# Optimization experiments

Hardware: AMD Instinct MI355X
Metric: run time of the kernel (lower is better)

The kernel has to match this reference:

```python
import jax, jax.numpy as jnp
import numpy as np

H = 1024   # hidden_dim
B = 4096   # batch
T = 128    # forecast_len
IN = 1     # output_dim (univariate)


def setup_inputs() -> dict:
    key = jax.random.key(0)
    ks = jax.random.split(key, 8)
    s = 1.0 / np.sqrt(H)  # torch LSTM/Linear default uniform init scale
    u = lambda k, shape: jax.random.uniform(k, shape, jnp.float32, -s, s)
    return {
        "hidden": jax.random.normal(ks[0], (1, B, H), jnp.float32),
        "cell":   jax.random.normal(ks[1], (1, B, H), jnp.float32),
        "W_ih":   u(ks[2], (4 * H, IN)),   # torch gate order: i, f, g, o
        "W_hh":   u(ks[3], (4 * H, H)),
        "b_ih":   u(ks[4], (4 * H,)),
        "b_hh":   u(ks[5], (4 * H,)),
        "W_out":  u(ks[6], (IN, H)),
        "b_out":  u(ks[7], (IN,)),
    }


def reference(hidden, cell, W_ih, W_hh, b_ih, b_hh, W_out, b_out):
    h = hidden[0]  # [B, H]  (num_layers == 1)
    c = cell[0]    # [B, H]
    x0 = jnp.zeros((h.shape[0], IN), h.dtype)  # initial decoder input = zeros
    b = b_ih + b_hh

    def step(carry, _):
        x, h, c = carry
        gates = x @ W_ih.T + h @ W_hh.T + b          # [B, 4H]
        i, f, g, o = jnp.split(gates, 4, axis=-1)    # torch order i,f,g,o
        c = jax.nn.sigmoid(f) * c + jax.nn.sigmoid(i) * jnp.tanh(g)
        h = jax.nn.sigmoid(o) * jnp.tanh(c)
        pred = h @ W_out.T + b_out                   # [B, 1]
        return (pred, h, c), pred                    # prediction fed back as next input

    _, preds = jax.lax.scan(step, (x0, h, c), None, length=T)  # [T, B, 1]
    return jnp.transpose(preds, (1, 0, 2))  # [B, T, 1]
```

## Files before the change

kernel.cpp:

```cpp
#include <hip/hip_runtime.h>
#include <hip/hip_bf16.h>
#include <stdint.h>


#define HH 1024
#define BB 4096
#define TT 128

#define BM 128
#define BN 256
#define BKK 32
#define NTIL 32

typedef __bf16 bf16;
typedef __bf16 v8bf __attribute__((ext_vector_type(8)));
typedef float f32x4 __attribute__((ext_vector_type(4)));

__device__ __forceinline__ float fast_sigmoid(float x) {
    return 1.0f / (1.0f + __expf(-x));
}
__device__ __forceinline__ float fast_tanh(float x) {
    return 1.0f - 2.0f / (__expf(2.0f * x) + 1.0f);
}

__device__ __forceinline__ void gload_lds16(const void* g, void* l) {
    __builtin_amdgcn_global_load_lds(
        (const __attribute__((address_space(1))) uint32_t*)(uintptr_t)g,
        (__attribute__((address_space(3))) uint32_t*)(uint32_t)(uintptr_t)l,
        16, 0, 0);
}

#define FENCE() asm volatile("" ::: "memory")
#define BAR() do { FENCE(); __builtin_amdgcn_s_barrier(); FENCE(); } while (0)
#define WAITV0() asm volatile("s_waitcnt vmcnt(0)" ::: "memory")
#define WAITV6() asm volatile("s_waitcnt vmcnt(6)" ::: "memory")
#define WAITL0() asm volatile("s_waitcnt lgkmcnt(0)" ::: "memory")


__global__ void prep_weights(const float* __restrict__ Whh,
                             const float* __restrict__ bih,
                             const float* __restrict__ bhh,
                             const float* __restrict__ Wih,
                             const float* __restrict__ Wout,
                             const float* __restrict__ bout,
                             bf16* __restrict__ Wr0, bf16* __restrict__ Wr1,
                             float* __restrict__ bias0, float* __restrict__ bias1) {
    int idx = blockIdx.x * blockDim.x + threadIdx.x;
    if (idx < 4 * HH * HH) {
        int k   = idx & (HH - 1);
        int row = idx >> 10;
        int jb2 = row >> 8;
        int g   = (row >> 6) & 3;
        int jj  = row & 63;
        int srow = g * HH + jb2 * 64 + jj;
        float wv = Whh[srow * HH + k];
        Wr0[idx] = (bf16)wv;
        Wr1[idx] = (bf16)(wv + Wih[srow] * Wout[k]);
    }
    if (idx < 4 * HH) {
        float b = bih[idx] + bhh[idx];
        bias0[idx] = b;
        bias1[idx] = b + Wih[idx] * bout[0];
    }
}

__global__ void prep_h(const float* __restrict__ h0, bf16* __restrict__ hb) {
    int idx = blockIdx.x * blockDim.x + threadIdx.x;
    if (idx < BB * HH) hb[idx] = (bf16)h0[idx];
}

__global__ void prep_c(const float* __restrict__ c0, bf16* __restrict__ cb) {
    int idx = blockIdx.x * blockDim.x + threadIdx.x;
    if (idx < BB * HH) cb[idx] = (bf16)c0[idx];
}

__global__ void prep_pred(float* __restrict__ predbuf, const float* __restrict__ b_out) {
    int idx = blockIdx.x * blockDim.x + threadIdx.x;
    if (idx < (TT + 1) * BB) predbuf[idx] = b_out[0];
}


#define STAGE1(SrcL, dstArr, TGT, ldsRowBase, KN)                              \
    gload_lds16((SrcL) + (size_t)(2 * (ldsRowBase)) * HH + (KN),               \
                &dstArr[TGT][ldsRowBase][0]);

#define READ_FRAGS(BUF)                                                        \
    _Pragma("unroll")                                                          \
    for (int mi = 0; mi < 4; mi++)                                             \
        a[mi] = *(const v8bf*)&As[BUF][waveM * 32 + mi * 8 + rh][pA];          \
    _Pragma("unroll")                                                          \
    for (int g = 0; g < 4; g++)                                                \
        _Pragma("unroll")                                                      \
        for (int jh = 0; jh < 2; jh++)                                         \
            b[g * 2 + jh] = *(const v8bf*)                                     \
                &Bs[BUF][g * 32 + waveN * 16 + jh * 8 + rh][pA];

#define MFMA_ALL()                                                             \
    __builtin_amdgcn_s_setprio(1);                                             \
    _Pragma("unroll")                                                          \
    for (int mi = 0; mi < 4; mi++)                                             \
        _Pragma("unroll")                                                      \
        for (int nt = 0; nt < 8; nt++)                                         \
            acc[mi][nt] = __builtin_amdgcn_mfma_f32_16x16x32_bf16(             \
                a[mi], b[nt], acc[mi][nt], 0, 0, 0);                           \
    __builtin_amdgcn_s_setprio(0);

#define TILE_BODY(BUF, TGT, T)                                                 \
    {                                                                          \
        v8bf a[4], b[8];                                                       \
        if ((T) < NTIL - 2) {                                                  \
            const int kn_ = ((T) + 2) * BKK;                                   \
            _Pragma("unroll")                                                  \
            for (int c2 = 0; c2 < 2; c2++)                                     \
                STAGE1(AsrcL, As, TGT, w * 16 + c2 * 8, kn_)                   \
            _Pragma("unroll")                                                  \
            for (int c2 = 0; c2 < 4; c2++)                                     \
                STAGE1(BsrcL, Bs, TGT, w * 32 + c2 * 8, kn_)                   \
        }                                                                      \
        READ_FRAGS(BUF)                                                        \
        MFMA_ALL()                                                             \
        WAITL0();                                                              \
        if ((T) < NTIL - 2) { WAITV6(); } else { WAITV0(); }                   \
        BAR();                                                                 \
    }

__global__ __launch_bounds__(256, 2)
void lstm_step(const bf16* __restrict__ hread, bf16* __restrict__ hwrite,
               bf16* __restrict__ cbuf,
               const bf16* __restrict__ Wr, const float* __restrict__ biasp,
               const float* __restrict__ Wout, float* __restrict__ predbuf_w) {
    __shared__ __align__(16) bf16 As[3][64][64];
    __shared__ __align__(16) bf16 Bs[3][128][64];

    const int tid   = threadIdx.x;
    const int lane  = tid & 63;
    const int w     = tid >> 6;
    const int waveM = w >> 1, waveN = w & 1;
    const int quad  = lane >> 4, l15 = lane & 15;

    const int bid    = blockIdx.x;
    const int jb2    = (bid & 7) * 2 + ((bid >> 3) & 1);
    const int blockB = (bid >> 4) * BM;

    const bf16* Asrc = hread + (size_t)blockB * HH;
    const bf16* Bsrc = Wr + (size_t)jb2 * 256 * HH;

    const int t1  = (lane & 7) ^ (lane >> 3);
    const int grl = 2 * (lane >> 3) + (t1 >> 2);
    const int c8  = (t1 & 3) * 8;
    const bf16* AsrcL = Asrc + (size_t)grl * HH + c8;
    const bf16* BsrcL = Bsrc + (size_t)grl * HH + c8;

    const int rh = l15 >> 1;
    const int pA = (((quad + 4 * (l15 & 1)) ^ rh)) * 8;

    float bsvv[2][4], wov[2];
#pragma unroll
    for (int jh = 0; jh < 2; jh++) {
        const int j = jb2 * 64 + waveN * 32 + jh * 16 + l15;
#pragma unroll
        for (int g = 0; g < 4; g++) bsvv[jh][g] = biasp[g * HH + j];
        wov[jh] = Wout[j];
    }

    f32x4 acc[4][8];
#pragma unroll
    for (int mi = 0; mi < 4; mi++)
#pragma unroll
        for (int g = 0; g < 4; g++)
#pragma unroll
            for (int jh = 0; jh < 2; jh++) {
                const float bv = bsvv[jh][g];
                acc[mi][g * 2 + jh] = (f32x4){bv, bv, bv, bv};
            }

#pragma unroll
    for (int c2 = 0; c2 < 2; c2++) STAGE1(AsrcL, As, 0, w * 16 + c2 * 8, 0)
#pragma unroll
    for (int c2 = 0; c2 < 4; c2++) STAGE1(BsrcL, Bs, 0, w * 32 + c2 * 8, 0)
#pragma unroll
    for (int c2 = 0; c2 < 2; c2++) STAGE1(AsrcL, As, 1, w * 16 + c2 * 8, BKK)
#pragma unroll
    for (int c2 = 0; c2 < 4; c2++) STAGE1(BsrcL, Bs, 1, w * 32 + c2 * 8, BKK)
    WAITV6();
    BAR();

#pragma unroll 1
    for (int tt = 0; tt < 10; tt++) {
        TILE_BODY(0, 2, 3 * tt)
        TILE_BODY(1, 0, 3 * tt + 1)
        TILE_BODY(2, 1, 3 * tt + 2)
    }
    TILE_BODY(0, 2, 30)
    TILE_BODY(1, 0, 31)

#pragma unroll
    for (int mi = 0; mi < 4; mi++) {
#pragma unroll
        for (int r = 0; r < 4; r++) {
            const int b = blockB + waveM * 64 + mi * 16 + quad * 4 + r;
            float pacc = 0.0f;
#pragma unroll
            for (int jh = 0; jh < 2; jh++) {
                const int j = jb2 * 64 + waveN * 32 + jh * 16 + l15;
                const float gi = acc[mi][0 + jh][r];
                const float gf = acc[mi][2 + jh][r];
                const float gg = acc[mi][4 + jh][r];
                const float go = acc[mi][6 + jh][r];
                const float cprev = (float)cbuf[(size_t)b * HH + j];
                const float cn = fast_sigmoid(gf) * cprev
                               + fast_sigmoid(gi) * fast_tanh(gg);
                cbuf[(size_t)b * HH + j] = (bf16)cn;
                const float hn = fast_sigmoid(go) * fast_tanh(cn);
                hwrite[(size_t)b * HH + j] = (bf16)hn;
                pacc += hn * wov[jh];
            }
            pacc += __shfl_xor(pacc, 1);
            pacc += __shfl_xor(pacc, 2);
            pacc += __shfl_xor(pacc, 4);
            pacc += __shfl_xor(pacc, 8);
            if (l15 == 0) atomicAdd(&predbuf_w[b], pacc);
        }
    }
}


__global__ void write_out(const float* __restrict__ predbuf, float* __restrict__ out) {
    int idx = blockIdx.x * blockDim.x + threadIdx.x;
    if (idx < BB * TT) {
        int t = idx & (TT - 1);
        int b = idx >> 7;
        out[idx] = predbuf[(size_t)(t + 1) * BB + b];
    }
}


extern "C" void kernel_launch(void* const* d_in, const int* in_sizes, int n_in,
                              void* d_out, int out_size, void* d_ws, size_t ws_size,
                              hipStream_t stream) {
    const float* hidden = (const float*)d_in[0];
    const float* cell   = (const float*)d_in[1];
    const float* Wih    = (const float*)d_in[2];
    const float* Whh    = (const float*)d_in[3];
    const float* bih    = (const float*)d_in[4];
    const float* bhh    = (const float*)d_in[5];
    const float* Wout   = (const float*)d_in[6];
    const float* bout   = (const float*)d_in[7];
    float* out = (float*)d_out;

    char* ws = (char*)d_ws;
    bf16* Wr0 = (bf16*)ws;       ws += (size_t)4 * HH * HH * 2;
    bf16* Wr1 = (bf16*)ws;       ws += (size_t)4 * HH * HH * 2;
    bf16* hb0 = (bf16*)ws;       ws += (size_t)BB * HH * 2;
    bf16* hb1 = (bf16*)ws;       ws += (size_t)BB * HH * 2;
    bf16* cbuf = (bf16*)ws;      ws += (size_t)BB * HH * 2;
    float* bias0 = (float*)ws;   ws += (size_t)4 * HH * 4;
    float* bias1 = (float*)ws;   ws += (size_t)4 * HH * 4;
    float* predbuf = (float*)ws; ws += (size_t)(TT + 1) * BB * 4;

    prep_weights<<<(4 * HH * HH + 255) / 256, 256, 0, stream>>>(
        Whh, bih, bhh, Wih, Wout, bout, Wr0, Wr1, bias0, bias1);
    prep_h<<<(BB * HH + 255) / 256, 256, 0, stream>>>(hidden, hb0);
    prep_c<<<(BB * HH + 255) / 256, 256, 0, stream>>>(cell, cbuf);
    prep_pred<<<((TT + 1) * BB + 255) / 256, 256, 0, stream>>>(predbuf, bout);

    bf16* hb[2] = {hb0, hb1};
    for (int t = 0; t < TT; t++) {
        const bf16* hr = hb[t & 1];
        bf16* hw = hb[(t + 1) & 1];
        const bf16* Wr   = (t == 0) ? Wr0 : Wr1;
        const float* bsp = (t == 0) ? bias0 : bias1;
        lstm_step<<<512, 256, 0, stream>>>(
            hr, hw, cbuf, Wr, bsp, Wout, predbuf + (size_t)(t + 1) * BB);
    }

    write_out<<<(BB * TT + 255) / 256, 256, 0, stream>>>(predbuf, out);
}
```

Baseline: 5.745 ms.

## Replace triple-buffered K pipeline with single-buffer BK=64 loop and new block mapping

```diff
diff --git a/kernel.cpp b/kernel.cpp
--- a/kernel.cpp
+++ b/kernel.cpp
@@ -8,9 +8,7 @@
 #define TT 128
 
 #define BM 128
-#define BN 256
-#define BKK 32
-#define NTIL 32
+#define BKK 64
 
 typedef __bf16 bf16;
 typedef __bf16 v8bf __attribute__((ext_vector_type(8)));
@@ -29,12 +27,6 @@
         (__attribute__((address_space(3))) uint32_t*)(uint32_t)(uintptr_t)l,
         16, 0, 0);
 }
-
-#define FENCE() asm volatile("" ::: "memory")
-#define BAR() do { FENCE(); __builtin_amdgcn_s_barrier(); FENCE(); } while (0)
-#define WAITV0() asm volatile("s_waitcnt vmcnt(0)" ::: "memory")
-#define WAITV6() asm volatile("s_waitcnt vmcnt(6)" ::: "memory")
-#define WAITL0() asm volatile("s_waitcnt lgkmcnt(0)" ::: "memory")
 
 
 __global__ void prep_weights(const float* __restrict__ Whh,
@@ -80,57 +72,13 @@
 }
 
 
-#define STAGE1(SrcL, dstArr, TGT, ldsRowBase, KN)                              \
-    gload_lds16((SrcL) + (size_t)(2 * (ldsRowBase)) * HH + (KN),               \
-                &dstArr[TGT][ldsRowBase][0]);
-
-#define READ_FRAGS(BUF)                                                        \
-    _Pragma("unroll")                                                          \
-    for (int mi = 0; mi < 4; mi++)                                             \
-        a[mi] = *(const v8bf*)&As[BUF][waveM * 32 + mi * 8 + rh][pA];          \
-    _Pragma("unroll")                                                          \
-    for (int g = 0; g < 4; g++)                                                \
-        _Pragma("unroll")                                                      \
-        for (int jh = 0; jh < 2; jh++)                                         \
-            b[g * 2 + jh] = *(const v8bf*)                                     \
-                &Bs[BUF][g * 32 + waveN * 16 + jh * 8 + rh][pA];
-
-#define MFMA_ALL()                                                             \
-    __builtin_amdgcn_s_setprio(1);                                             \
-    _Pragma("unroll")                                                          \
-    for (int mi = 0; mi < 4; mi++)                                             \
-        _Pragma("unroll")                                                      \
-        for (int nt = 0; nt < 8; nt++)                                         \
-            acc[mi][nt] = __builtin_amdgcn_mfma_f32_16x16x32_bf16(             \
-                a[mi], b[nt], acc[mi][nt], 0, 0, 0);                           \
-    __builtin_amdgcn_s_setprio(0);
-
-#define TILE_BODY(BUF, TGT, T)                                                 \
-    {                                                                          \
-        v8bf a[4], b[8];                                                       \
-        if ((T) < NTIL - 2) {                                                  \
-            const int kn_ = ((T) + 2) * BKK;                                   \
-            _Pragma("unroll")                                                  \
-            for (int c2 = 0; c2 < 2; c2++)                                     \
-                STAGE1(AsrcL, As, TGT, w * 16 + c2 * 8, kn_)                   \
-            _Pragma("unroll")                                                  \
-            for (int c2 = 0; c2 < 4; c2++)                                     \
-                STAGE1(BsrcL, Bs, TGT, w * 32 + c2 * 8, kn_)                   \
-        }                                                                      \
-        READ_FRAGS(BUF)                                                        \
-        MFMA_ALL()                                                             \
-        WAITL0();                                                              \
-        if ((T) < NTIL - 2) { WAITV6(); } else { WAITV0(); }                   \
-        BAR();                                                                 \
-    }
-
 __global__ __launch_bounds__(256, 2)
 void lstm_step(const bf16* __restrict__ hread, bf16* __restrict__ hwrite,
                bf16* __restrict__ cbuf,
                const bf16* __restrict__ Wr, const float* __restrict__ biasp,
                const float* __restrict__ Wout, float* __restrict__ predbuf_w) {
-    __shared__ __align__(16) bf16 As[3][64][64];
-    __shared__ __align__(16) bf16 Bs[3][128][64];
+    __shared__ bf16 As[BM][BKK];
+    __shared__ bf16 Bs[2 * BM][BKK];
 
     const int tid   = threadIdx.x;
     const int lane  = tid & 63;
@@ -138,21 +86,17 @@
     const int waveM = w >> 1, waveN = w & 1;
     const int quad  = lane >> 4, l15 = lane & 15;
 
-    const int bid    = blockIdx.x;
-    const int jb2    = (bid & 7) * 2 + ((bid >> 3) & 1);
-    const int blockB = (bid >> 4) * BM;
+    const int bid = blockIdx.x;
+    const int xcd = bid & 7, loc = bid >> 3;
+    const int jb2 = (xcd & 3) * 4 + (loc & 3);
+    const int blockB = ((xcd >> 2) * 16 + (loc >> 2)) * BM;
 
     const bf16* Asrc = hread + (size_t)blockB * HH;
     const bf16* Bsrc = Wr + (size_t)jb2 * 256 * HH;
 
-    const int t1  = (lane & 7) ^ (lane >> 3);
-    const int grl = 2 * (lane >> 3) + (t1 >> 2);
-    const int c8  = (t1 & 3) * 8;
-    const bf16* AsrcL = Asrc + (size_t)grl * HH + c8;
-    const bf16* BsrcL = Bsrc + (size_t)grl * HH + c8;
-
-    const int rh = l15 >> 1;
-    const int pA = (((quad + 4 * (l15 & 1)) ^ rh)) * 8;
+    const int r8  = lane >> 3;
+    const int gc  = (lane & 7) ^ r8;
+    const int swr = l15 & 7;
 
     float bsvv[2][4], wov[2];
 #pragma unroll
@@ -174,25 +118,41 @@
                 acc[mi][g * 2 + jh] = (f32x4){bv, bv, bv, bv};
             }
 
-#pragma unroll
-    for (int c2 = 0; c2 < 2; c2++) STAGE1(AsrcL, As, 0, w * 16 + c2 * 8, 0)
-#pragma unroll
-    for (int c2 = 0; c2 < 4; c2++) STAGE1(BsrcL, Bs, 0, w * 32 + c2 * 8, 0)
-#pragma unroll
-    for (int c2 = 0; c2 < 2; c2++) STAGE1(AsrcL, As, 1, w * 16 + c2 * 8, BKK)
-#pragma unroll
-    for (int c2 = 0; c2 < 4; c2++) STAGE1(BsrcL, Bs, 1, w * 32 + c2 * 8, BKK)
-    WAITV6();
-    BAR();
-
-#pragma unroll 1
-    for (int tt = 0; tt < 10; tt++) {
-        TILE_BODY(0, 2, 3 * tt)
-        TILE_BODY(1, 0, 3 * tt + 1)
-        TILE_BODY(2, 1, 3 * tt + 2)
-    }
-    TILE_BODY(0, 2, 30)
-    TILE_BODY(1, 0, 31)
+    for (int k0 = 0; k0 < HH; k0 += BKK) {
+#pragma unroll
+        for (int c2 = 0; c2 < 4; c2++) {
+            const int rowb = w * 32 + c2 * 8;
+            gload_lds16(Asrc + (size_t)(rowb + r8) * HH + k0 + gc * 8, &As[rowb][0]);
+        }
+#pragma unroll
+        for (int c2 = 0; c2 < 8; c2++) {
+            const int rowb = w * 64 + c2 * 8;
+            gload_lds16(Bsrc + (size_t)(rowb + r8) * HH + k0 + gc * 8, &Bs[rowb][0]);
+        }
+        asm volatile("s_waitcnt vmcnt(0)" ::: "memory");
+        __syncthreads();
+#pragma unroll
+        for (int kk = 0; kk < 2; kk++) {
+            v8bf a[4], b[8];
+            const int pch = ((kk * 4 + quad) ^ swr) * 8;
+#pragma unroll
+            for (int mi = 0; mi < 4; mi++)
+                a[mi] = *(const v8bf*)&As[waveM * 64 + mi * 16 + l15][pch];
+#pragma unroll
+            for (int g = 0; g < 4; g++)
+#pragma unroll
+                for (int jh = 0; jh < 2; jh++)
+                    b[g * 2 + jh] =
+                        *(const v8bf*)&Bs[g * 64 + waveN * 32 + jh * 16 + l15][pch];
+#pragma unroll
+            for (int mi = 0; mi < 4; mi++)
+#pragma unroll
+                for (int nt = 0; nt < 8; nt++)
+                    acc[mi][nt] = __builtin_amdgcn_mfma_f32_16x16x32_bf16(
+                        a[mi], b[nt], acc[mi][nt], 0, 0, 0);
+        }
+        __syncthreads();
+    }
 
 #pragma unroll
     for (int mi = 0; mi < 4; mi++) {
```

After: 5.156 ms (median of 2 runs). 10.2% less time.
